# Kernel tuning notes

Measured on AMD Instinct MI355X. Metric: run time of the kernel, lower is better.

The kernel has to match this reference:

```python
import jax, jax.numpy as jnp
import numpy as np

B, T, F_, H1, H2, HEADS = 64, 128, 64, 32, 64, 4
E = H2 * F_  # embed_dim = hidden_dims[-1] * feats = 4096


def conv2d(x, w, b):
    # x: [b,c,H,W], w: [o,c,kh,kw], SAME padding (kernel 3 -> pad 1)
    y = jax.lax.conv_general_dilated(x, w, (1, 1), 'SAME',
                                     dimension_numbers=('NCHW', 'OIHW', 'NCHW'))
    return y + b[None, :, None, None]


def gru_layer(xs, h0, wg, bg, wc, bc):
    # xs: [b,t,c,H,W]; h0: [b,h,H,W]. Standard ConvGRU cell:
    #   r,u = sigmoid(conv([x,h])); cand = tanh(conv([x, r*h]))
    #   h' = (1-u)*h + u*cand
    def step(h, x):
        g = conv2d(jnp.concatenate([x, h], axis=1), wg, bg)
        r, u = jnp.split(jax.nn.sigmoid(g), 2, axis=1)
        cand = jnp.tanh(conv2d(jnp.concatenate([x, r * h], axis=1), wc, bc))
        h_next = (1.0 - u) * h + u * cand
        return h_next, h_next
    hT, ys = jax.lax.scan(step, h0, jnp.swapaxes(xs, 0, 1))
    return jnp.swapaxes(ys, 0, 1), hT  # [b,t,h,H,W], [b,h,H,W]


def mha(q, k, v, w_qkv, b_qkv, w_out, b_out):
    # q: [b,1,E], k/v: [b,t,E]; torch nn.MultiheadAttention (eval, no dropout)
    wq, wk, wv = jnp.split(w_qkv, 3, axis=0)
    bq, bk, bv = jnp.split(b_qkv, 3, axis=0)
    dh = E // HEADS
    def heads(x, w, bb):
        y = x @ w.T + bb
        b_, l_, _ = y.shape
        return y.reshape(b_, l_, HEADS, dh).transpose(0, 2, 1, 3)  # [b,h,l,dh]
    qh, kh, vh = heads(q, wq, bq), heads(k, wk, bk), heads(v, wv, bv)
    scores = jnp.einsum('bhqd,bhkd->bhqk', qh, kh) / jnp.sqrt(jnp.float32(dh))
    attn = jax.nn.softmax(scores, axis=-1)
    ctx = jnp.einsum('bhqk,bhkd->bhqd', attn, vh)
    ctx = ctx.transpose(0, 2, 1, 3).reshape(q.shape[0], q.shape[1], E)
    return ctx @ w_out.T + b_out


def setup_inputs() -> dict:
    key = jax.random.key(0)
    ks = jax.random.split(key, 24)
    s = 0.05
    d = {'x': jax.random.normal(ks[0], (B, T, F_), dtype=jnp.float32)}
    # encoder layer 0: in=1, h=H1; layer 1: in=H1, h=H2
    d['wg_e0'] = jax.random.normal(ks[1], (2 * H1, 1 + H1, 3, 3)) * s
    d['bg_e0'] = jnp.zeros((2 * H1,))
    d['wc_e0'] = jax.random.normal(ks[2], (H1, 1 + H1, 3, 3)) * s
    d['bc_e0'] = jnp.zeros((H1,))
    d['wg_e1'] = jax.random.normal(ks[3], (2 * H2, H1 + H2, 3, 3)) * s
    d['bg_e1'] = jnp.zeros((2 * H2,))
    d['wc_e1'] = jax.random.normal(ks[4], (H2, H1 + H2, 3, 3)) * s
    d['bc_e1'] = jnp.zeros((H2,))
    # decoder: input dim = 2*H2; hidden dims reversed [H2, H1]
    d['wg_d0'] = jax.random.normal(ks[5], (2 * H2, 2 * H2 + H2, 3, 3)) * s
    d['bg_d0'] = jnp.zeros((2 * H2,))
    d['wc_d0'] = jax.random.normal(ks[6], (H2, 2 * H2 + H2, 3, 3)) * s
    d['bc_d0'] = jnp.zeros((H2,))
    d['wg_d1'] = jax.random.normal(ks[7], (2 * H1, H2 + H1, 3, 3)) * s
    d['bg_d1'] = jnp.zeros((2 * H1,))
    d['wc_d1'] = jax.random.normal(ks[8], (H1, H2 + H1, 3, 3)) * s
    d['bc_d1'] = jnp.zeros((H1,))
    d['w_qkv'] = jax.random.normal(ks[9], (3 * E, E)) * (1.0 / np.sqrt(E))
    d['b_qkv'] = jnp.zeros((3 * E,))
    d['w_out'] = jax.random.normal(ks[10], (E, E)) * (1.0 / np.sqrt(E))
    d['b_out'] = jnp.zeros((E,))
    d['w_fin'] = jax.random.normal(ks[11], (1, H1, 1, 1)) * s
    d['b_fin'] = jnp.zeros((1,))
    return d


def reference(x, wg_e0, bg_e0, wc_e0, bc_e0, wg_e1, bg_e1, wc_e1, bc_e1,
              wg_d0, bg_d0, wc_d0, bc_d0, wg_d1, bg_d1, wc_d1, bc_d1,
              w_qkv, b_qkv, w_out, b_out, w_fin, b_fin):
    b, t, f = x.shape
    xr = x.reshape(b, t, 1, f, 1)
    # encoder (2 ConvGRU layers, zero init states)
    y0, h0 = gru_layer(xr, jnp.zeros((b, H1, f, 1), x.dtype), wg_e0, bg_e0, wc_e0, bc_e0)
    y1, h1 = gru_layer(y0, jnp.zeros((b, H2, f, 1), x.dtype), wg_e1, bg_e1, wc_e1, bc_e1)
    # attention bottleneck: query = last hidden, memory = encoder outputs
    query = h1.reshape(b, 1, E)
    memory = y1.reshape(b, t, E)
    context = mha(query, memory, memory, w_qkv, b_qkv, w_out, b_out)  # [b,1,E]
    ctx = context.reshape(b, 1, H2, f, 1)
    dec_in = jnp.concatenate([y1, jnp.broadcast_to(ctx, (b, t, H2, f, 1))], axis=2)
    # decoder init states: encoder last states reversed -> [h1 (H2), h0 (H1)]
    z0, _ = gru_layer(dec_in, h1, wg_d0, bg_d0, wc_d0, bc_d0)
    z1, _ = gru_layer(z0, h0, wg_d1, bg_d1, wc_d1, bc_d1)  # [b,t,H1,f,1]
    # final 1x1 conv applied per timestep == channel contraction
    rec = jnp.einsum('btcfw,oc->btofw', z1, w_fin[:, :, 0, 0]) + b_fin[None, None, :, None, None]
    return rec.reshape(b, t, f)
```

## Files before the change

kernel.cpp:

```cpp
#include <hip/hip_runtime.h>
#include <cstdint>


#define B_  64
#define T_  128
#define TC  32
#define NCH 4

__device__ __forceinline__ float wsum(float v) {
#pragma unroll
  for (int m = 32; m > 0; m >>= 1) v += __shfl_xor(v, m, 64);
  return v;
}
__device__ __forceinline__ float wmaxr(float v) {
#pragma unroll
  for (int m = 32; m > 0; m >>= 1) v = fmaxf(v, __shfl_xor(v, m, 64));
  return v;
}
__device__ __forceinline__ float sigmoidf_(float x) {
  return 1.f / (1.f + __expf(-x));
}
__device__ __forceinline__ float tanhf_(float x) {
  x = fminf(fmaxf(x, -15.f), 15.f);
  float e2 = __expf(2.f * x);
  return (e2 - 1.f) / (e2 + 1.f);
}

struct PackArgs {
  const float* src[16];
  float* dst[16];
  int intot[16];
  int ic0[16];
  int icn[16];
  int oc[16];
};

__global__ __launch_bounds__(256) void pack_all_kernel(PackArgs pa) {
  const int j = blockIdx.y;
  const int icN = pa.icn[j];
  const int total = pa.oc[j] * icN * 3;
  const int i = blockIdx.x * 256 + threadIdx.x;
  if (i >= total) return;
  const int per_oc = icN * 3;
  const int oc = i / per_oc;
  const int rem = i - oc * per_oc;
  const int ic = rem / 3, dk = rem - ic * 3;
  pa.dst[j][i] =
      pa.src[j][((size_t)(oc * pa.intot[j] + pa.ic0[j] + ic) * 3 + dk) * 3 + 1];
}

template <int INC, int OG, int OCC>
__device__ __forceinline__ void conv_x_body(
    float (*sin_)[72], int tid, int btl,
    const float* __restrict__ seq, int seqC, size_t sB,
    const float* __restrict__ ctx,
    const float* __restrict__ Wgx, const float* __restrict__ Wcx,
    const float* __restrict__ bg, const float* __restrict__ bc,
    float* __restrict__ out) {
  constexpr int OCT = OG + OCC;
  constexpr int NJ = OG / 32;
  constexpr int NJC = OCC / 32;
  const int b = btl >> 5;
  const int tl = btl & 31;
  const int ocg = tid >> 3;
  const int f0 = (tid & 7) << 3;

  for (int idx = tid; idx < INC * 72; idx += 256) {
    int ic = idx / 72, ff = idx - ic * 72;
    float v = 0.f;
    if (ff >= 1 && ff <= 64) {
      int fs = ff - 1;
      v = (ic < seqC)
              ? seq[(size_t)b * sB + (size_t)tl * seqC * 64 + ic * 64 + fs]
              : ctx[((size_t)b * (INC - seqC) + (ic - seqC)) * 64 + fs];
    }
    sin_[ic][ff] = v;
  }
  __syncthreads();

  if constexpr (INC >= 4) {
    {
      float acc[NJ][8];
#pragma unroll
      for (int j = 0; j < NJ; ++j) {
        float bb = bg[ocg + 32 * j];
#pragma unroll
        for (int ff = 0; ff < 8; ++ff) acc[j][ff] = bb;
      }
      for (int ic0 = 0; ic0 < INC; ic0 += 4) {
        float hv[4][10];
#pragma unroll
        for (int q = 0; q < 4; ++q) {
          float4 a4 = *(const float4*)&sin_[ic0 + q][f0];
          float4 b4 = *(const float4*)&sin_[ic0 + q][f0 + 4];
          float2 c2 = *(const float2*)&sin_[ic0 + q][f0 + 8];
          hv[q][0] = a4.x; hv[q][1] = a4.y; hv[q][2] = a4.z; hv[q][3] = a4.w;
          hv[q][4] = b4.x; hv[q][5] = b4.y; hv[q][6] = b4.z; hv[q][7] = b4.w;
          hv[q][8] = c2.x; hv[q][9] = c2.y;
        }
#pragma unroll
        for (int j = 0; j < NJ; ++j) {
          const int oc = ocg + 32 * j;
          const float4* w4 = (const float4*)(Wgx + ((size_t)oc * INC + ic0) * 3);
          float4 wa = w4[0], wb = w4[1], wc4 = w4[2];
          const float wt[12] = {wa.x, wa.y, wa.z, wa.w, wb.x, wb.y, wb.z, wb.w,
                                wc4.x, wc4.y, wc4.z, wc4.w};
#pragma unroll
          for (int q = 0; q < 4; ++q) {
            const float w0 = wt[3 * q], w1 = wt[3 * q + 1], w2 = wt[3 * q + 2];
#pragma unroll
            for (int ff = 0; ff < 8; ++ff)
              acc[j][ff] = fmaf(w0, hv[q][ff], fmaf(w1, hv[q][ff + 1], fmaf(w2, hv[q][ff + 2], acc[j][ff])));
          }
        }
      }
#pragma unroll
      for (int j = 0; j < NJ; ++j) {
        float* dst = out + ((size_t)btl * OCT + ocg + 32 * j) * 64 + f0;
        *(float4*)dst = make_float4(acc[j][0], acc[j][1], acc[j][2], acc[j][3]);
        *(float4*)(dst + 4) = make_float4(acc[j][4], acc[j][5], acc[j][6], acc[j][7]);
      }
    }
    {
      float acc[NJC][8];
#pragma unroll
      for (int j = 0; j < NJC; ++j) {
        float bb = bc[ocg + 32 * j];
#pragma unroll
        for (int ff = 0; ff < 8; ++ff) acc[j][ff] = bb;
      }
      for (int ic0 = 0; ic0 < INC; ic0 += 4) {
        float hv[4][10];
#pragma unroll
        for (int q = 0; q < 4; ++q) {
          float4 a4 = *(const float4*)&sin_[ic0 + q][f0];
          float4 b4 = *(const float4*)&sin_[ic0 + q][f0 + 4];
          float2 c2 = *(const float2*)&sin_[ic0 + q][f0 + 8];
          hv[q][0] = a4.x; hv[q][1] = a4.y; hv[q][2] = a4.z; hv[q][3] = a4.w;
          hv[q][4] = b4.x; hv[q][5] = b4.y; hv[q][6] = b4.z; hv[q][7] = b4.w;
          hv[q][8] = c2.x; hv[q][9] = c2.y;
        }
#pragma unroll
        for (int j = 0; j < NJC; ++j) {
          const int oc = ocg + 32 * j;
          const float4* w4 = (const float4*)(Wcx + ((size_t)oc * INC + ic0) * 3);
          float4 wa = w4[0], wb = w4[1], wc4 = w4[2];
          const float wt[12] = {wa.x, wa.y, wa.z, wa.w, wb.x, wb.y, wb.z, wb.w,
                                wc4.x, wc4.y, wc4.z, wc4.w};
#pragma unroll
          for (int q = 0; q < 4; ++q) {
            const float w0 = wt[3 * q], w1 = wt[3 * q + 1], w2 = wt[3 * q + 2];
#pragma unroll
            for (int ff = 0; ff < 8; ++ff)
              acc[j][ff] = fmaf(w0, hv[q][ff], fmaf(w1, hv[q][ff + 1], fmaf(w2, hv[q][ff + 2], acc[j][ff])));
          }
        }
      }
#pragma unroll
      for (int j = 0; j < NJC; ++j) {
        float* dst = out + ((size_t)btl * OCT + OG + ocg + 32 * j) * 64 + f0;
        *(float4*)dst = make_float4(acc[j][0], acc[j][1], acc[j][2], acc[j][3]);
        *(float4*)(dst + 4) = make_float4(acc[j][4], acc[j][5], acc[j][6], acc[j][7]);
      }
    }
  } else {
    float hv[10];
    {
      float4 a4 = *(const float4*)&sin_[0][f0];
      float4 b4 = *(const float4*)&sin_[0][f0 + 4];
      float2 c2 = *(const float2*)&sin_[0][f0 + 8];
      hv[0] = a4.x; hv[1] = a4.y; hv[2] = a4.z; hv[3] = a4.w;
      hv[4] = b4.x; hv[5] = b4.y; hv[6] = b4.z; hv[7] = b4.w;
      hv[8] = c2.x; hv[9] = c2.y;
    }
#pragma unroll
    for (int j = 0; j < NJ; ++j) {
      const int oc = ocg + 32 * j;
      const float w0 = Wgx[oc * 3], w1 = Wgx[oc * 3 + 1], w2 = Wgx[oc * 3 + 2];
      float acc[8];
#pragma unroll
      for (int ff = 0; ff < 8; ++ff)
        acc[ff] = fmaf(w0, hv[ff], fmaf(w1, hv[ff + 1], fmaf(w2, hv[ff + 2], bg[oc])));
      float* dst = out + ((size_t)btl * OCT + oc) * 64 + f0;
      *(float4*)dst = make_float4(acc[0], acc[1], acc[2], acc[3]);
      *(float4*)(dst + 4) = make_float4(acc[4], acc[5], acc[6], acc[7]);
    }
#pragma unroll
    for (int j = 0; j < NJC; ++j) {
      const int oc = ocg + 32 * j;
      const float w0 = Wcx[oc * 3], w1 = Wcx[oc * 3 + 1], w2 = Wcx[oc * 3 + 2];
      float acc[8];
#pragma unroll
      for (int ff = 0; ff < 8; ++ff)
        acc[ff] = fmaf(w0, hv[ff], fmaf(w1, hv[ff + 1], fmaf(w2, hv[ff + 2], bc[oc])));
      float* dst = out + ((size_t)btl * OCT + OG + oc) * 64 + f0;
      *(float4*)dst = make_float4(acc[0], acc[1], acc[2], acc[3]);
      *(float4*)(dst + 4) = make_float4(acc[4], acc[5], acc[6], acc[7]);
    }
  }
}

template <int INC, int OG, int OCC>
__global__ __launch_bounds__(256) void conv_x_kernel(
    const float* __restrict__ seq, int seqC, size_t sB,
    const float* __restrict__ ctx,
    const float* __restrict__ Wgx, const float* __restrict__ Wcx,
    const float* __restrict__ bg, const float* __restrict__ bc,
    float* __restrict__ out) {
  __shared__ float sin_[INC][72];
  conv_x_body<INC, OG, OCC>(sin_, threadIdx.x, blockIdx.x, seq, seqC, sB, ctx,
                            Wgx, Wcx, bg, bc, out);
}

__device__ __forceinline__ void final_body(
    int tid, int tile, const float* __restrict__ z1c,
    const float* __restrict__ wfin, const float* __restrict__ bfin,
    float* __restrict__ out, int tOff) {
  const int idx = tile * 256 + tid;
  const int f = idx & 63;
  const int tl = (idx >> 6) & 31;
  const int b = idx >> 11;
  const float* zp = z1c + ((size_t)b * TC + tl) * 2048 + f;
  float a = bfin[0];
#pragma unroll
  for (int c = 0; c < 32; ++c) a = fmaf(wfin[c], zp[c * 64], a);
  out[(size_t)b * 8192 + (size_t)(tOff + tl) * 64 + f] = a;
}

__global__ __launch_bounds__(256) void final_kernel(
    const float* __restrict__ z1c,
    const float* __restrict__ wfin, const float* __restrict__ bfin,
    float* __restrict__ out, int tOff) {
  final_body(threadIdx.x, blockIdx.x, z1c, wfin, bfin, out, tOff);
}

template <int HC>
__device__ __forceinline__ void gru_body(
    float* smem,
    const float* __restrict__ A, const float* __restrict__ Wgh,
    const float* __restrict__ Wch, const float* hinit,
    float* __restrict__ Y, size_t yB, float* hfinal, int b) {
  constexpr int NR = HC / 32;
  constexpr int OG = 2 * HC;
  constexpr int OCT = 3 * HC;
  float(*Hs)[68] = (float(*)[68])smem;
  float(*Rs)[68] = (float(*)[68])(smem + HC * 68);
  const int tid = threadIdx.x;
  const int ocg = tid >> 4;
  const int f0 = (tid & 15) << 2;
  const int im = (f0 == 0) ? 0 : f0 - 1;
  const bool lo = (f0 == 0), hi = (f0 == 60);

  float hreg[NR][4];
#pragma unroll
  for (int r = 0; r < NR; ++r) {
    const int oc = ocg + 32 * r;
    const float4 v = *(const float4*)(hinit + ((size_t)b * HC + oc) * 64 + f0);
    hreg[r][0] = v.x; hreg[r][1] = v.y; hreg[r][2] = v.z; hreg[r][3] = v.w;
    *(float4*)&Hs[oc][f0] = v;
  }
  __syncthreads();
  __builtin_amdgcn_s_setprio(1);

  for (int tl = 0; tl < TC; ++tl) {
    const float* Abt = A + ((size_t)b * TC + tl) * (OCT * 64);
    float accr[NR][4], accu[NR][4], accc[NR][4];
#pragma unroll
    for (int r = 0; r < NR; ++r) {
      const int oc = ocg + 32 * r;
      const float4 vr = *(const float4*)(Abt + (size_t)oc * 64 + f0);
      const float4 vu = *(const float4*)(Abt + (size_t)(HC + oc) * 64 + f0);
      const float4 vc = *(const float4*)(Abt + (size_t)(OG + oc) * 64 + f0);
      accr[r][0] = vr.x; accr[r][1] = vr.y; accr[r][2] = vr.z; accr[r][3] = vr.w;
      accu[r][0] = vu.x; accu[r][1] = vu.y; accu[r][2] = vu.z; accu[r][3] = vu.w;
      accc[r][0] = vc.x; accc[r][1] = vc.y; accc[r][2] = vc.z; accc[r][3] = vc.w;
    }
#pragma unroll 2
    for (int hc0 = 0; hc0 < HC; hc0 += 4) {
      float hv[4][6];
#pragma unroll
      for (int q = 0; q < 4; ++q) {
        const float4 h4 = *(const float4*)&Hs[hc0 + q][f0];
        const float lf = Hs[hc0 + q][im];
        const float rt = Hs[hc0 + q][f0 + 4];
        hv[q][0] = lo ? 0.f : lf;
        hv[q][1] = h4.x; hv[q][2] = h4.y; hv[q][3] = h4.z; hv[q][4] = h4.w;
        hv[q][5] = hi ? 0.f : rt;
      }
#pragma unroll
      for (int r = 0; r < NR; ++r) {
        {
          const float4* w4 = (const float4*)(Wgh + ((size_t)(ocg + 32 * r) * HC + hc0) * 3);
          const float4 wa = w4[0], wb = w4[1], wc4 = w4[2];
          const float wt[12] = {wa.x, wa.y, wa.z, wa.w, wb.x, wb.y, wb.z, wb.w,
                                wc4.x, wc4.y, wc4.z, wc4.w};
#pragma unroll
          for (int q = 0; q < 4; ++q) {
            const float w0 = wt[3 * q], w1 = wt[3 * q + 1], w2 = wt[3 * q + 2];
#pragma unroll
            for (int ff = 0; ff < 4; ++ff)
              accr[r][ff] = fmaf(w0, hv[q][ff], fmaf(w1, hv[q][ff + 1], fmaf(w2, hv[q][ff + 2], accr[r][ff])));
          }
        }
        {
          const float4* w4 = (const float4*)(Wgh + ((size_t)(HC + ocg + 32 * r) * HC + hc0) * 3);
          const float4 wa = w4[0], wb = w4[1], wc4 = w4[2];
          const float wt[12] = {wa.x, wa.y, wa.z, wa.w, wb.x, wb.y, wb.z, wb.w,
                                wc4.x, wc4.y, wc4.z, wc4.w};
#pragma unroll
          for (int q = 0; q < 4; ++q) {
            const float w0 = wt[3 * q], w1 = wt[3 * q + 1], w2 = wt[3 * q + 2];
#pragma unroll
            for (int ff = 0; ff < 4; ++ff)
              accu[r][ff] = fmaf(w0, hv[q][ff], fmaf(w1, hv[q][ff + 1], fmaf(w2, hv[q][ff + 2], accu[r][ff])));
          }
        }
      }
    }
// ... 11 lines not shown
    __syncthreads();
#pragma unroll 2
    for (int hc0 = 0; hc0 < HC; hc0 += 4) {
      float hv[4][6];
#pragma unroll
      for (int q = 0; q < 4; ++q) {
        const float4 h4 = *(const float4*)&Rs[hc0 + q][f0];
        const float lf = Rs[hc0 + q][im];
        const float rt = Rs[hc0 + q][f0 + 4];
        hv[q][0] = lo ? 0.f : lf;
        hv[q][1] = h4.x; hv[q][2] = h4.y; hv[q][3] = h4.z; hv[q][4] = h4.w;
        hv[q][5] = hi ? 0.f : rt;
      }
#pragma unroll
      for (int r = 0; r < NR; ++r) {
        const float4* w4 = (const float4*)(Wch + ((size_t)(ocg + 32 * r) * HC + hc0) * 3);
        const float4 wa = w4[0], wb = w4[1], wc4 = w4[2];
        const float wt[12] = {wa.x, wa.y, wa.z, wa.w, wb.x, wb.y, wb.z, wb.w,
                              wc4.x, wc4.y, wc4.z, wc4.w};
#pragma unroll
        for (int q = 0; q < 4; ++q) {
          const float w0 = wt[3 * q], w1 = wt[3 * q + 1], w2 = wt[3 * q + 2];
#pragma unroll
          for (int ff = 0; ff < 4; ++ff)
            accc[r][ff] = fmaf(w0, hv[q][ff], fmaf(w1, hv[q][ff + 1], fmaf(w2, hv[q][ff + 2], accc[r][ff])));
        }
      }
    }
#pragma unroll
    for (int r = 0; r < NR; ++r) {
      const int oc = ocg + 32 * r;
      float4 yv;
#pragma unroll
      for (int ff = 0; ff < 4; ++ff) {
        const float cd = tanhf_(accc[r][ff]);
        const float hn = fmaf(uu[r][ff], cd - hreg[r][ff], hreg[r][ff]);
        hreg[r][ff] = hn;
        (&yv.x)[ff] = hn;
      }
      *(float4*)(Y + (size_t)b * yB + (size_t)tl * (HC * 64) + (size_t)oc * 64 + f0) = yv;
      *(float4*)&Hs[oc][f0] = yv;
    }
    __syncthreads();
  }
  __builtin_amdgcn_s_setprio(0);
#pragma unroll
  for (int r = 0; r < NR; ++r) {
    const int oc = ocg + 32 * r;
    *(float4*)(hfinal + ((size_t)b * HC + oc) * 64 + f0) =
        make_float4(hreg[r][0], hreg[r][1], hreg[r][2], hreg[r][3]);
  }
}

template <int HC>
__global__ __launch_bounds__(512) void gru_rec_kernel(
    const float* __restrict__ A, const float* __restrict__ Wgh,
    const float* __restrict__ Wch, const float* hinit,
    float* __restrict__ Y, size_t yB, float* hfinal) {
  __shared__ float smem[2 * HC * 68];
  gru_body<HC>(smem, A, Wgh, Wch, hinit, Y, yB, hfinal, blockIdx.x);
}

struct GruArgs {
  const float* A;
  const float* Wgh;
  const float* Wch;
  const float* hinit;
  float* Y;
  size_t yB;
  float* hfinal;
};

__global__ __launch_bounds__(512) void gru_fused_kernel(GruArgs g64, GruArgs g32) {
  __shared__ float smem[2 * 64 * 68];
  if (blockIdx.x < 64) {
    gru_body<64>(smem, g64.A, g64.Wgh, g64.Wch, g64.hinit, g64.Y, g64.yB,
                 g64.hfinal, blockIdx.x);
  } else {
    gru_body<32>(smem, g32.A, g32.Wgh, g32.Wch, g32.hinit, g32.Y, g32.yB,
                 g32.hfinal, blockIdx.x - 64);
  }
}

struct ConvJob {
  int kind;
  int nblk;
  const float* seq;
  int seqC;
  size_t sB;
  const float* ctx;
  const float* w0;
  const float* w1;
  const float* b0;
  const float* b1;
  float* out;
  int tOff;
};

struct MegaArgs {
  GruArgs g64;
  GruArgs g32;
  int ng64, ng32, njobs;
  ConvJob jobs[4];
};

__global__ __launch_bounds__(512) void mega_kernel(MegaArgs ma) {
  __shared__ float smem[18432];
  int bid = blockIdx.x;
  if (bid < ma.ng64) {
    gru_body<64>(smem, ma.g64.A, ma.g64.Wgh, ma.g64.Wch, ma.g64.hinit,
                 ma.g64.Y, ma.g64.yB, ma.g64.hfinal, bid);
    return;
  }
  bid -= ma.ng64;
  if (bid < ma.ng32) {
    gru_body<32>(smem, ma.g32.A, ma.g32.Wgh, ma.g32.Wch, ma.g32.hinit,
                 ma.g32.Y, ma.g32.yB, ma.g32.hfinal, bid);
    return;
  }
  bid -= ma.ng32;
  const int half = threadIdx.x >> 8;
  const int tid = threadIdx.x & 255;
#pragma unroll 1
  for (int j = 0; j < ma.njobs; ++j) {
    if (bid < ma.jobs[j].nblk) {
      const ConvJob cj = ma.jobs[j];
      const int tile = bid * 2 + half;
      if (cj.kind == 2) {
        conv_x_body<128, 128, 64>((float(*)[72])(smem + half * 128 * 72), tid,
                                  tile, cj.seq, cj.seqC, cj.sB, cj.ctx, cj.w0,
                                  cj.w1, cj.b0, cj.b1, cj.out);
      } else if (cj.kind == 3) {
        conv_x_body<64, 64, 32>((float(*)[72])(smem + half * 64 * 72), tid,
                                tile, cj.seq, cj.seqC, cj.sB, cj.ctx, cj.w0,
                                cj.w1, cj.b0, cj.b1, cj.out);
      } else {
        final_body(tid, tile, cj.seq, cj.w0, cj.b0, cj.out, cj.tOff);
      }
      return;
    }
    bid -= ma.jobs[j].nblk;
  }
}

template <bool WT>
__global__ __launch_bounds__(256) void gemm64_kernel(
    const float* __restrict__ W, int wrs,
    const float* __restrict__ X, int xrs,
    float* __restrict__ O, int ors,
    const float* __restrict__ bias, int K,
    int ebh, size_t hsW, size_t hsX, size_t hsO, size_t hsB) {
  int eb = blockIdx.x;
  if (ebh > 0) {
    int h = blockIdx.x / ebh;
    eb = blockIdx.x - h * ebh;
    W += h * hsW; X += h * hsX; O += h * hsO;
    if (bias) bias += h * hsB;
  }
  const int e0 = eb * 64;
  __shared__ float Xs[64][68];
  __shared__ float Ws[64][68];
  const int tb4 = (threadIdx.x & 15) << 2;
  const int te4 = (threadIdx.x >> 4) << 2;
  float acc[4][4] = {};
  for (int k0 = 0; k0 < K; k0 += 64) {
    {
      const int row = threadIdx.x >> 2;
      const int kq = (threadIdx.x & 3) << 4;
      const float* src = X + (size_t)row * xrs + k0 + kq;
#pragma unroll
      for (int q = 0; q < 4; ++q) {
        float4 v = *(const float4*)(src + (q << 2));
        Xs[kq + (q << 2) + 0][row] = v.x;
        Xs[kq + (q << 2) + 1][row] = v.y;
        Xs[kq + (q << 2) + 2][row] = v.z;
        Xs[kq + (q << 2) + 3][row] = v.w;
      }
    }
    if (!WT) {
      const int row = threadIdx.x >> 2;
      const int kq = (threadIdx.x & 3) << 4;
      const float* src = W + (size_t)(e0 + row) * wrs + k0 + kq;
#pragma unroll
      for (int q = 0; q < 4; ++q) {
        float4 v = *(const float4*)(src + (q << 2));
        Ws[kq + (q << 2) + 0][row] = v.x;
        Ws[kq + (q << 2) + 1][row] = v.y;
        Ws[kq + (q << 2) + 2][row] = v.z;
// ... 86 lines not shown
  const int e = eb * 256 + threadIdx.x;
  __shared__ float ap[4][128];
  for (int i = threadIdx.x; i < 512; i += 256)
    ap[i >> 7][i & 127] = attnp[(size_t)b * 512 + i];
  __syncthreads();
  float a0 = 0, a1 = 0, a2 = 0, a3 = 0;
  const float* mb = mem + (size_t)b * 128 * 4096 + e;
#pragma unroll 4
  for (int t = 0; t < 128; ++t) {
    float m = mb[(size_t)t * 4096];
    a0 = fmaf(ap[0][t], m, a0);
    a1 = fmaf(ap[1][t], m, a1);
    a2 = fmaf(ap[2][t], m, a2);
    a3 = fmaf(ap[3][t], m, a3);
  }
  wmem[((size_t)b * 4 + 0) * 4096 + e] = a0;
  wmem[((size_t)b * 4 + 1) * 4096 + e] = a1;
  wmem[((size_t)b * 4 + 2) * 4096 + e] = a2;
  wmem[((size_t)b * 4 + 3) * 4096 + e] = a3;
}

extern "C" void kernel_launch(void* const* d_in, const int* in_sizes, int n_in,
                              void* d_out, int out_size, void* d_ws, size_t ws_size,
                              hipStream_t stream) {
  (void)in_sizes; (void)n_in; (void)out_size;
  const float* x     = (const float*)d_in[0];
  const float* wg_e0 = (const float*)d_in[1];
  const float* bg_e0 = (const float*)d_in[2];
  const float* wc_e0 = (const float*)d_in[3];
  const float* bc_e0 = (const float*)d_in[4];
  const float* wg_e1 = (const float*)d_in[5];
  const float* bg_e1 = (const float*)d_in[6];
  const float* wc_e1 = (const float*)d_in[7];
  const float* bc_e1 = (const float*)d_in[8];
  const float* wg_d0 = (const float*)d_in[9];
  const float* bg_d0 = (const float*)d_in[10];
  const float* wc_d0 = (const float*)d_in[11];
  const float* bc_d0 = (const float*)d_in[12];
  const float* wg_d1 = (const float*)d_in[13];
  const float* bg_d1 = (const float*)d_in[14];
  const float* wc_d1 = (const float*)d_in[15];
  const float* bc_d1 = (const float*)d_in[16];
  const float* w_qkv = (const float*)d_in[17];
  const float* b_qkv = (const float*)d_in[18];
  const float* w_out = (const float*)d_in[19];
  const float* b_out = (const float*)d_in[20];
  const float* w_fin = (const float*)d_in[21];
  const float* b_fin = (const float*)d_in[22];
  float* out = (float*)d_out;

  float* WS = (float*)d_ws;
  size_t off = 0;
  auto alloc = [&](size_t n) { float* p = WS + off; off += (n + 63) & ~(size_t)63; return p; };
  float* Amp0 = alloc((size_t)B_ * TC * 192 * 64);
  float* A960 = alloc((size_t)B_ * TC * 96 * 64);
  float* Y0c  = alloc((size_t)B_ * TC * 32 * 64);
  float* Y1   = alloc((size_t)B_ * T_ * 64 * 64);
  float* Z0p[2] = {alloc((size_t)B_ * TC * 64 * 64), alloc((size_t)B_ * TC * 64 * 64)};
  float* Z1p0 = alloc((size_t)B_ * TC * 32 * 64);
  float* He0p[2] = {alloc((size_t)B_ * 32 * 64), alloc((size_t)B_ * 32 * 64)};
  float* He1p[2] = {alloc((size_t)B_ * 64 * 64), alloc((size_t)B_ * 64 * 64)};
  float* Hd0p[2] = {alloc((size_t)B_ * 64 * 64), alloc((size_t)B_ * 64 * 64)};
  float* Hd1p[2] = {alloc((size_t)B_ * 32 * 64), alloc((size_t)B_ * 32 * 64)};
  float* QBUF = alloc((size_t)B_ * 4096);
  float* QKH  = alloc((size_t)B_ * 4 * 4096);
  float* WMEM = alloc((size_t)B_ * 4 * 4096);
  float* CTXB = alloc((size_t)B_ * 4096);
  float* CTXO = alloc((size_t)B_ * 4096);
  float* SCR  = alloc((size_t)B_ * 4 * 128);
  float* ATTN = alloc((size_t)B_ * 4 * 128);
  float* wgx_e0 = alloc(64 * 1 * 3);    float* wgh_e0 = alloc(64 * 32 * 3);
  float* wcx_e0 = alloc(32 * 1 * 3);    float* wch_e0 = alloc(32 * 32 * 3);
  float* wgx_e1 = alloc(128 * 32 * 3);  float* wgh_e1 = alloc(128 * 64 * 3);
  float* wcx_e1 = alloc(64 * 32 * 3);   float* wch_e1 = alloc(64 * 64 * 3);
  float* wgx_d0 = alloc(128 * 128 * 3); float* wgh_d0 = alloc(128 * 64 * 3);
  float* wcx_d0 = alloc(64 * 128 * 3);  float* wch_d0 = alloc(64 * 64 * 3);
  float* wgx_d1 = alloc(64 * 64 * 3);   float* wgh_d1 = alloc(64 * 32 * 3);
  float* wcx_d1 = alloc(32 * 64 * 3);   float* wch_d1 = alloc(32 * 32 * 3);
  const size_t off_r9 = off;
  float* Amp1 = alloc((size_t)B_ * TC * 192 * 64);
  float* A961 = alloc((size_t)B_ * TC * 96 * 64);
  float* Z1p1 = alloc((size_t)B_ * TC * 32 * 64);
  const size_t off_full = off;
  if (ws_size < off_r9 * sizeof(float)) return;
  const bool mega_ok = (ws_size >= off_full * sizeof(float));

  float* Amp[2] = {Amp0, Amp1};
  float* A96p[2] = {A960, A961};
  float* Z1p[2] = {Z1p0, Z1p1};

  {
    PackArgs pa;
    const float* srcs[16] = {wg_e0, wg_e0, wc_e0, wc_e0, wg_e1, wg_e1, wc_e1, wc_e1,
                             wg_d0, wg_d0, wc_d0, wc_d0, wg_d1, wg_d1, wc_d1, wc_d1};
    float* dsts[16] = {wgx_e0, wgh_e0, wcx_e0, wch_e0, wgx_e1, wgh_e1, wcx_e1, wch_e1,
                       wgx_d0, wgh_d0, wcx_d0, wch_d0, wgx_d1, wgh_d1, wcx_d1, wch_d1};
    int intot[16] = {33, 33, 33, 33, 96, 96, 96, 96, 192, 192, 192, 192, 96, 96, 96, 96};
    int ic0[16]   = {0, 1, 0, 1, 0, 32, 0, 32, 0, 128, 0, 128, 0, 64, 0, 64};
    int icn[16]   = {1, 32, 1, 32, 32, 64, 32, 64, 128, 64, 128, 64, 64, 32, 64, 32};
    int occ[16]   = {64, 64, 32, 32, 128, 128, 64, 64, 128, 128, 64, 64, 64, 64, 32, 32};
    for (int j = 0; j < 16; ++j) {
      pa.src[j] = srcs[j]; pa.dst[j] = dsts[j];
      pa.intot[j] = intot[j]; pa.ic0[j] = ic0[j]; pa.icn[j] = icn[j]; pa.oc[j] = occ[j];
    }
    pack_all_kernel<<<dim3(192, 16), 256, 0, stream>>>(pa);
  }

  hipMemsetAsync(He0p[0], 0, (size_t)B_ * 32 * 64 * 4, stream);
  hipMemsetAsync(He1p[0], 0, (size_t)B_ * 64 * 64 * 4, stream);

  auto conv_e0 = [&](int c) {
    conv_x_kernel<1, 64, 32><<<2048, 256, 0, stream>>>(
        x + (size_t)c * TC * 64, 1, (size_t)T_ * 64, nullptr,
        wgx_e0, wcx_e0, bg_e0, bc_e0, A96p[0]);
  };
  auto conv_e1 = [&]() {
    conv_x_kernel<32, 128, 64><<<2048, 256, 0, stream>>>(
        Y0c, 32, (size_t)TC * 32 * 64, nullptr,
        wgx_e1, wcx_e1, bg_e1, bc_e1, Amp[0]);
  };

  conv_e0(0);
  gru_rec_kernel<32><<<64, 512, 0, stream>>>(
      A96p[0], wgh_e0, wch_e0, He0p[0], Y0c, (size_t)TC * 2048, He0p[1]);
  conv_e1();
  for (int c = 0; c < NCH; ++c) {
    GruArgs g64 = {Amp[0], wgh_e1, wch_e1, He1p[c & 1],
                   Y1 + (size_t)c * TC * 4096, (size_t)T_ * 4096, He1p[(c + 1) & 1]};
    if (c < NCH - 1) {
      conv_e0(c + 1);
      GruArgs g32 = {A96p[0], wgh_e0, wch_e0, He0p[(c + 1) & 1],
                     Y0c, (size_t)TC * 2048, He0p[c & 1]};
      gru_fused_kernel<<<128, 512, 0, stream>>>(g64, g32);
      conv_e1();
    } else {
      gru_rec_kernel<64><<<64, 512, 0, stream>>>(
          g64.A, g64.Wgh, g64.Wch, g64.hinit, g64.Y, g64.yB, g64.hfinal);
    }
  }
  float* He0f = He0p[0];
  float* He1f = He1p[0];

  const float* wq = w_qkv;
  const float* wk = w_qkv + (size_t)4096 * 4096;
  const float* wv = w_qkv + (size_t)8192 * 4096;
  gemm64_kernel<false><<<64, 256, 0, stream>>>(wq, 4096, He1f, 4096, QBUF, 4096,
                                               b_qkv, 4096, 0, 0, 0, 0, 0);
  gemm64_kernel<true><<<256, 256, 0, stream>>>(wk, 4096, QBUF, 4096, QKH, 16384,
                                               nullptr, 1024, 64,
                                               (size_t)1024 * 4096, 1024, 4096, 0);
  attn_scores_kernel<<<B_ * 16, 256, 0, stream>>>(QKH, Y1, SCR);
  attn_softmax_kernel<<<B_, 256, 0, stream>>>(SCR, QBUF, b_qkv, ATTN);
  attn_wsum_kernel<<<B_ * 16, 256, 0, stream>>>(ATTN, Y1, WMEM);
  gemm64_kernel<false><<<64, 256, 0, stream>>>(wv, 4096, WMEM, 16384, CTXB, 4096,
                                               b_qkv + 8192, 4096, 16,
                                               (size_t)1024 * 4096, 4096, 1024, 1024);
  gemm64_kernel<false><<<64, 256, 0, stream>>>(w_out, 4096, CTXB, 4096, CTXO, 4096,
                                               b_out, 4096, 0, 0, 0, 0, 0);

  if (mega_ok) {
    auto JD0 = [&](int c, float* dst) {
      ConvJob j{}; j.kind = 2; j.nblk = 1024;
      j.seq = Y1 + (size_t)c * TC * 4096; j.seqC = 64; j.sB = (size_t)T_ * 4096;
      j.ctx = CTXO; j.w0 = wgx_d0; j.w1 = wcx_d0; j.b0 = bg_d0; j.b1 = bc_d0;
      j.out = dst; return j;
    };
    auto JD1 = [&](float* z0src, float* dst) {
      ConvJob j{}; j.kind = 3; j.nblk = 1024;
      j.seq = z0src; j.seqC = 64; j.sB = (size_t)TC * 4096;
      j.ctx = nullptr; j.w0 = wgx_d1; j.w1 = wcx_d1; j.b0 = bg_d1; j.b1 = bc_d1;
      j.out = dst; return j;
    };
    auto JFIN = [&](float* z1src, int tOff) {
      ConvJob j{}; j.kind = 4; j.nblk = 256;
      j.seq = z1src; j.w0 = w_fin; j.b0 = b_fin; j.out = out; j.tOff = tOff;
      return j;
    };
    auto mega = [&](const GruArgs* a64, const GruArgs* a32, int nj,
                    const ConvJob* js) {
      MegaArgs ma{};
      ma.ng64 = a64 ? 64 : 0; if (a64) ma.g64 = *a64;
      ma.ng32 = a32 ? 64 : 0; if (a32) ma.g32 = *a32;
      ma.njobs = nj;
      int grid = ma.ng64 + ma.ng32;
      for (int i = 0; i < nj; ++i) { ma.jobs[i] = js[i]; grid += js[i].nblk; }
      mega_kernel<<<grid, 512, 0, stream>>>(ma);
    };

    GruArgs gd0[4], gd1[4];
    for (int c = 0; c < 4; ++c) {
      gd0[c] = {Amp[c & 1], wgh_d0, wch_d0,
                (c == 0 ? He1f : Hd0p[c & 1]),
                Z0p[c & 1], (size_t)TC * 4096, Hd0p[(c + 1) & 1]};
      gd1[c] = {A96p[c & 1], wgh_d1, wch_d1,
                (c == 0 ? He0f : Hd1p[c & 1]),
                Z1p[c & 1], (size_t)TC * 2048, Hd1p[(c + 1) & 1]};
    }

    conv_x_kernel<128, 128, 64><<<2048, 256, 0, stream>>>(
        Y1, 64, (size_t)T_ * 4096, CTXO, wgx_d0, wcx_d0, bg_d0, bc_d0, Amp[0]);
    { ConvJob js[1] = {JD0(1, Amp[1])};
      mega(&gd0[0], nullptr, 1, js); }
    { ConvJob js[2] = {JD1(Z0p[0], A96p[0]), JD0(2, Amp[0])};
      mega(&gd0[1], nullptr, 2, js); }
    { ConvJob js[2] = {JD1(Z0p[1], A96p[1]), JD0(3, Amp[1])};
      mega(&gd0[2], &gd1[0], 2, js); }
    { ConvJob js[2] = {JD1(Z0p[0], A96p[0]), JFIN(Z1p[0], 0)};
      mega(&gd0[3], &gd1[1], 2, js); }
    { ConvJob js[2] = {JD1(Z0p[1], A96p[1]), JFIN(Z1p[1], TC)};
      mega(nullptr, &gd1[2], 2, js); }
    { ConvJob js[1] = {JFIN(Z1p[0], 2 * TC)};
      mega(nullptr, &gd1[3], 1, js); }
    final_kernel<<<512, 256, 0, stream>>>(Z1p[1], w_fin, b_fin, out, 3 * TC);
  } else {
    auto conv_d0 = [&](int c) {
      conv_x_kernel<128, 128, 64><<<2048, 256, 0, stream>>>(
          Y1 + (size_t)c * TC * 4096, 64, (size_t)T_ * 4096, CTXO,
          wgx_d0, wcx_d0, bg_d0, bc_d0, Amp[0]);
    };
    auto conv_d1 = [&](int c) {
      conv_x_kernel<64, 64, 32><<<2048, 256, 0, stream>>>(
          Z0p[c & 1], 64, (size_t)TC * 4096, nullptr,
          wgx_d1, wcx_d1, bg_d1, bc_d1, A96p[0]);
    };
    conv_d0(0);
    gru_rec_kernel<64><<<64, 512, 0, stream>>>(
        Amp[0], wgh_d0, wch_d0, He1f, Z0p[0], (size_t)TC * 4096, Hd0p[1]);
    conv_d1(0);
    for (int c = 1; c < NCH; ++c) {
      conv_d0(c);
      GruArgs g64 = {Amp[0], wgh_d0, wch_d0, Hd0p[c & 1],
                     Z0p[c & 1], (size_t)TC * 4096, Hd0p[(c + 1) & 1]};
      GruArgs g32 = {A96p[0], wgh_d1, wch_d1,
                     (c - 1 == 0 ? He0f : Hd1p[(c - 1) & 1]),
                     Z1p[0], (size_t)TC * 2048, Hd1p[c & 1]};
      gru_fused_kernel<<<128, 512, 0, stream>>>(g64, g32);
      final_kernel<<<512, 256, 0, stream>>>(Z1p[0], w_fin, b_fin, out, (c - 1) * TC);
      conv_d1(c);
    }
    gru_rec_kernel<32><<<64, 512, 0, stream>>>(
        A96p[0], wgh_d1, wch_d1, Hd1p[1], Z1p[0], (size_t)TC * 2048, Hd1p[0]);
    final_kernel<<<512, 256, 0, stream>>>(Z1p[0], w_fin, b_fin, out, 3 * TC);
  }
}
```

Measured before the change: 7.725 ms.

## Halve time-chunk size and generalize mega-kernel pipeline over more chunks

Reduces the time chunk from 32 to 16 steps (8 chunks) and turns the hand-written decoder mega-kernel schedule into a generic software pipeline. GRU recurrence, input convolutions and the final projection of adjacent chunks now overlap in each launch. The encoder layer-0 input convolution is hoisted into one full-sequence launch, and buffers are double-buffered unconditionally. The aim is a shorter pipeline fill/drain so the serial GRU chain is less exposed, at the cost of more launches and a larger workspace requirement.

New measurement: 7.282 ms, median of 2. 1.06x faster.

```diff
diff --git a/kernel.cpp b/kernel.cpp
--- a/kernel.cpp
+++ b/kernel.cpp
@@ -4,8 +4,8 @@
 
 #define B_  64
 #define T_  128
-#define TC  32
-#define NCH 4
+#define TC  16
+#define NCH 8
 
 __device__ __forceinline__ float wsum(float v) {
 #pragma unroll
@@ -51,7 +51,7 @@
 
 template <int INC, int OG, int OCC>
 __device__ __forceinline__ void conv_x_body(
-    float (*sin_)[72], int tid, int btl,
+    float (*sin_)[72], int tid, int b, int tl, int oidx,
     const float* __restrict__ seq, int seqC, size_t sB,
     const float* __restrict__ ctx,
     const float* __restrict__ Wgx, const float* __restrict__ Wcx,
@@ -60,8 +60,6 @@
   constexpr int OCT = OG + OCC;
   constexpr int NJ = OG / 32;
   constexpr int NJC = OCC / 32;
-  const int b = btl >> 5;
-  const int tl = btl & 31;
   const int ocg = tid >> 3;
   const int f0 = (tid & 7) << 3;
 
@@ -116,7 +114,7 @@
       }
 #pragma unroll
       for (int j = 0; j < NJ; ++j) {
-        float* dst = out + ((size_t)btl * OCT + ocg + 32 * j) * 64 + f0;
+        float* dst = out + ((size_t)oidx * OCT + ocg + 32 * j) * 64 + f0;
         *(float4*)dst = make_float4(acc[j][0], acc[j][1], acc[j][2], acc[j][3]);
         *(float4*)(dst + 4) = make_float4(acc[j][4], acc[j][5], acc[j][6], acc[j][7]);
       }
@@ -158,7 +156,7 @@
       }
 #pragma unroll
       for (int j = 0; j < NJC; ++j) {
-        float* dst = out + ((size_t)btl * OCT + OG + ocg + 32 * j) * 64 + f0;
+        float* dst = out + ((size_t)oidx * OCT + OG + ocg + 32 * j) * 64 + f0;
         *(float4*)dst = make_float4(acc[j][0], acc[j][1], acc[j][2], acc[j][3]);
         *(float4*)(dst + 4) = make_float4(acc[j][4], acc[j][5], acc[j][6], acc[j][7]);
       }
@@ -181,7 +179,7 @@
 #pragma unroll
       for (int ff = 0; ff < 8; ++ff)
         acc[ff] = fmaf(w0, hv[ff], fmaf(w1, hv[ff + 1], fmaf(w2, hv[ff + 2], bg[oc])));
-      float* dst = out + ((size_t)btl * OCT + oc) * 64 + f0;
+      float* dst = out + ((size_t)oidx * OCT + oc) * 64 + f0;
       *(float4*)dst = make_float4(acc[0], acc[1], acc[2], acc[3]);
       *(float4*)(dst + 4) = make_float4(acc[4], acc[5], acc[6], acc[7]);
     }
@@ -193,7 +191,7 @@
 #pragma unroll
       for (int ff = 0; ff < 8; ++ff)
         acc[ff] = fmaf(w0, hv[ff], fmaf(w1, hv[ff + 1], fmaf(w2, hv[ff + 2], bc[oc])));
-      float* dst = out + ((size_t)btl * OCT + OG + oc) * 64 + f0;
+      float* dst = out + ((size_t)oidx * OCT + OG + oc) * 64 + f0;
       *(float4*)dst = make_float4(acc[0], acc[1], acc[2], acc[3]);
       *(float4*)(dst + 4) = make_float4(acc[4], acc[5], acc[6], acc[7]);
     }
@@ -206,10 +204,12 @@
     const float* __restrict__ ctx,
     const float* __restrict__ Wgx, const float* __restrict__ Wcx,
     const float* __restrict__ bg, const float* __restrict__ bc,
-    float* __restrict__ out) {
+    float* __restrict__ out, int tdiv) {
   __shared__ float sin_[INC][72];
-  conv_x_body<INC, OG, OCC>(sin_, threadIdx.x, blockIdx.x, seq, seqC, sB, ctx,
-                            Wgx, Wcx, bg, bc, out);
+  const int b = blockIdx.x / tdiv;
+  const int tl = blockIdx.x - b * tdiv;
+  conv_x_body<INC, OG, OCC>(sin_, threadIdx.x, b, tl, blockIdx.x, seq, seqC,
+                            sB, ctx, Wgx, Wcx, bg, bc, out);
 }
 
 __device__ __forceinline__ void final_body(
@@ -218,8 +218,8 @@
     float* __restrict__ out, int tOff) {
   const int idx = tile * 256 + tid;
   const int f = idx & 63;
-  const int tl = (idx >> 6) & 31;
-  const int b = idx >> 11;
+  const int tl = (idx >> 6) & (TC - 1);
+  const int b = idx >> 10;
   const float* zp = z1c + ((size_t)b * TC + tl) * 2048 + f;
   float a = bfin[0];
 #pragma unroll
@@ -237,8 +237,9 @@
 template <int HC>
 __device__ __forceinline__ void gru_body(
     float* smem,
-    const float* __restrict__ A, const float* __restrict__ Wgh,
-    const float* __restrict__ Wch, const float* hinit,
+    const float* __restrict__ A, size_t aB,
+    const float* __restrict__ Wgh, const float* __restrict__ Wch,
+    const float* hinit,
     float* __restrict__ Y, size_t yB, float* hfinal, int b) {
   constexpr int NR = HC / 32;
   constexpr int OG = 2 * HC;
@@ -263,7 +264,7 @@
   __builtin_amdgcn_s_setprio(1);
 
   for (int tl = 0; tl < TC; ++tl) {
-    const float* Abt = A + ((size_t)b * TC + tl) * (OCT * 64);
+    const float* Abt = A + (size_t)b * aB + (size_t)tl * (OCT * 64);
     float accr[NR][4], accu[NR][4], accc[NR][4];
 #pragma unroll
     for (int r = 0; r < NR; ++r) {
@@ -381,17 +382,9 @@
   }
 }
 
-template <int HC>
-__global__ __launch_bounds__(512) void gru_rec_kernel(
-    const float* __restrict__ A, const float* __restrict__ Wgh,
-    const float* __restrict__ Wch, const float* hinit,
-    float* __restrict__ Y, size_t yB, float* hfinal) {
-  __shared__ float smem[2 * HC * 68];
-  gru_body<HC>(smem, A, Wgh, Wch, hinit, Y, yB, hfinal, blockIdx.x);
-}
-
 struct GruArgs {
   const float* A;
+  size_t aB;
   const float* Wgh;
   const float* Wch;
   const float* hinit;
@@ -400,14 +393,21 @@
   float* hfinal;
 };
 
+template <int HC>
+__global__ __launch_bounds__(512) void gru_rec_kernel(GruArgs g) {
+  __shared__ float smem[2 * HC * 68];
+  gru_body<HC>(smem, g.A, g.aB, g.Wgh, g.Wch, g.hinit, g.Y, g.yB, g.hfinal,
+               blockIdx.x);
+}
+
 __global__ __launch_bounds__(512) void gru_fused_kernel(GruArgs g64, GruArgs g32) {
   __shared__ float smem[2 * 64 * 68];
   if (blockIdx.x < 64) {
-    gru_body<64>(smem, g64.A, g64.Wgh, g64.Wch, g64.hinit, g64.Y, g64.yB,
-                 g64.hfinal, blockIdx.x);
+    gru_body<64>(smem, g64.A, g64.aB, g64.Wgh, g64.Wch, g64.hinit, g64.Y,
+                 g64.yB, g64.hfinal, blockIdx.x);
   } else {
-    gru_body<32>(smem, g32.A, g32.Wgh, g32.Wch, g32.hinit, g32.Y, g32.yB,
-                 g32.hfinal, blockIdx.x - 64);
+    gru_body<32>(smem, g32.A, g32.aB, g32.Wgh, g32.Wch, g32.hinit, g32.Y,
+                 g32.yB, g32.hfinal, blockIdx.x - 64);
   }
 }
 
@@ -437,14 +437,14 @@
   __shared__ float smem[18432];
   int bid = blockIdx.x;
   if (bid < ma.ng64) {
-    gru_body<64>(smem, ma.g64.A, ma.g64.Wgh, ma.g64.Wch, ma.g64.hinit,
-                 ma.g64.Y, ma.g64.yB, ma.g64.hfinal, bid);
+    gru_body<64>(smem, ma.g64.A, ma.g64.aB, ma.g64.Wgh, ma.g64.Wch,
+                 ma.g64.hinit, ma.g64.Y, ma.g64.yB, ma.g64.hfinal, bid);
     return;
   }
   bid -= ma.ng64;
   if (bid < ma.ng32) {
-    gru_body<32>(smem, ma.g32.A, ma.g32.Wgh, ma.g32.Wch, ma.g32.hinit,
-                 ma.g32.Y, ma.g32.yB, ma.g32.hfinal, bid);
+    gru_body<32>(smem, ma.g32.A, ma.g32.aB, ma.g32.Wgh, ma.g32.Wch,
+                 ma.g32.hinit, ma.g32.Y, ma.g32.yB, ma.g32.hfinal, bid);
     return;
   }
   bid -= ma.ng32;
@@ -455,14 +455,16 @@
     if (bid < ma.jobs[j].nblk) {
       const ConvJob cj = ma.jobs[j];
       const int tile = bid * 2 + half;
+      const int b = tile >> 4;
+      const int tl = tile & (TC - 1);
       if (cj.kind == 2) {
         conv_x_body<128, 128, 64>((float(*)[72])(smem + half * 128 * 72), tid,
-                                  tile, cj.seq, cj.seqC, cj.sB, cj.ctx, cj.w0,
-                                  cj.w1, cj.b0, cj.b1, cj.out);
+                                  b, tl, tile, cj.seq, cj.seqC, cj.sB, cj.ctx,
+                                  cj.w0, cj.w1, cj.b0, cj.b1, cj.out);
       } else if (cj.kind == 3) {
         conv_x_body<64, 64, 32>((float(*)[72])(smem + half * 64 * 72), tid,
-                                tile, cj.seq, cj.seqC, cj.sB, cj.ctx, cj.w0,
-                                cj.w1, cj.b0, cj.b1, cj.out);
+                                b, tl, tile, cj.seq, cj.seqC, cj.sB, cj.ctx,
+                                cj.w0, cj.w1, cj.b0, cj.b1, cj.out);
       } else {
         final_body(tid, tile, cj.seq, cj.w0, cj.b0, cj.out, cj.tOff);
       }
@@ -655,12 +657,13 @@
   float* WS = (float*)d_ws;
   size_t off = 0;
   auto alloc = [&](size_t n) { float* p = WS + off; off += (n + 63) & ~(size_t)63; return p; };
-  float* Amp0 = alloc((size_t)B_ * TC * 192 * 64);
-  float* A960 = alloc((size_t)B_ * TC * 96 * 64);
-  float* Y0c  = alloc((size_t)B_ * TC * 32 * 64);
+  float* Amp[2] = {alloc((size_t)B_ * TC * 192 * 64), alloc((size_t)B_ * TC * 192 * 64)};
+  float* A96full = alloc((size_t)B_ * T_ * 96 * 64);
+  float* A96d[2] = {alloc((size_t)B_ * TC * 96 * 64), alloc((size_t)B_ * TC * 96 * 64)};
+  float* Y0p[2] = {alloc((size_t)B_ * TC * 32 * 64), alloc((size_t)B_ * TC * 32 * 64)};
   float* Y1   = alloc((size_t)B_ * T_ * 64 * 64);
   float* Z0p[2] = {alloc((size_t)B_ * TC * 64 * 64), alloc((size_t)B_ * TC * 64 * 64)};
-  float* Z1p0 = alloc((size_t)B_ * TC * 32 * 64);
+  float* Z1p[2] = {alloc((size_t)B_ * TC * 32 * 64), alloc((size_t)B_ * TC * 32 * 64)};
   float* He0p[2] = {alloc((size_t)B_ * 32 * 64), alloc((size_t)B_ * 32 * 64)};
   float* He1p[2] = {alloc((size_t)B_ * 64 * 64), alloc((size_t)B_ * 64 * 64)};
   float* Hd0p[2] = {alloc((size_t)B_ * 64 * 64), alloc((size_t)B_ * 64 * 64)};
@@ -680,17 +683,7 @@
   float* wcx_d0 = alloc(64 * 128 * 3);  float* wch_d0 = alloc(64 * 64 * 3);
   float* wgx_d1 = alloc(64 * 64 * 3);   float* wgh_d1 = alloc(64 * 32 * 3);
   float* wcx_d1 = alloc(32 * 64 * 3);   float* wch_d1 = alloc(32 * 32 * 3);
-  const size_t off_r9 = off;
-  float* Amp1 = alloc((size_t)B_ * TC * 192 * 64);
-  float* A961 = alloc((size_t)B_ * TC * 96 * 64);
-  float* Z1p1 = alloc((size_t)B_ * TC * 32 * 64);
-  const size_t off_full = off;
-  if (ws_size < off_r9 * sizeof(float)) return;
-  const bool mega_ok = (ws_size >= off_full * sizeof(float));
-
-  float* Amp[2] = {Amp0, Amp1};
-  float* A96p[2] = {A960, A961};
-  float* Z1p[2] = {Z1p0, Z1p1};
+  if (ws_size < off * sizeof(float)) return;
 
   {
     PackArgs pa;
@@ -712,33 +705,34 @@
   hipMemsetAsync(He0p[0], 0, (size_t)B_ * 32 * 64 * 4, stream);
   hipMemsetAsync(He1p[0], 0, (size_t)B_ * 64 * 64 * 4, stream);
 
-  auto conv_e0 = [&](int c) {
-    conv_x_kernel<1, 64, 32><<<2048, 256, 0, stream>>>(
-        x + (size_t)c * TC * 64, 1, (size_t)T_ * 64, nullptr,
-        wgx_e0, wcx_e0, bg_e0, bc_e0, A96p[0]);
+  conv_x_kernel<1, 64, 32><<<B_ * T_, 256, 0, stream>>>(
+      x, 1, (size_t)T_ * 64, nullptr, wgx_e0, wcx_e0, bg_e0, bc_e0,
+      A96full, T_);
+
+  auto g32e = [&](int c) {
+    GruArgs g{A96full + (size_t)c * TC * 96 * 64, (size_t)T_ * 96 * 64,
+              wgh_e0, wch_e0, He0p[c & 1], Y0p[c & 1], (size_t)TC * 2048,
+              He0p[(c + 1) & 1]};
+    return g;
   };
-  auto conv_e1 = [&]() {
-    conv_x_kernel<32, 128, 64><<<2048, 256, 0, stream>>>(
-        Y0c, 32, (size_t)TC * 32 * 64, nullptr,
-        wgx_e1, wcx_e1, bg_e1, bc_e1, Amp[0]);
+  auto conv_e1 = [&](int c) {
+    conv_x_kernel<32, 128, 64><<<B_ * TC, 256, 0, stream>>>(
+        Y0p[c & 1], 32, (size_t)TC * 2048, nullptr,
+        wgx_e1, wcx_e1, bg_e1, bc_e1, Amp[c & 1], TC);
   };
 
-  conv_e0(0);
-  gru_rec_kernel<32><<<64, 512, 0, stream>>>(
-      A96p[0], wgh_e0, wch_e0, He0p[0], Y0c, (size_t)TC * 2048, He0p[1]);
-  conv_e1();
+  { GruArgs g = g32e(0); gru_rec_kernel<32><<<64, 512, 0, stream>>>(g); }
+  conv_e1(0);
   for (int c = 0; c < NCH; ++c) {
-    GruArgs g64 = {Amp[0], wgh_e1, wch_e1, He1p[c & 1],
-                   Y1 + (size_t)c * TC * 4096, (size_t)T_ * 4096, He1p[(c + 1) & 1]};
+    GruArgs g64 = {Amp[c & 1], (size_t)TC * 192 * 64, wgh_e1, wch_e1,
+                   He1p[c & 1], Y1 + (size_t)c * TC * 4096, (size_t)T_ * 4096,
+                   He1p[(c + 1) & 1]};
     if (c < NCH - 1) {
-      conv_e0(c + 1);
-      GruArgs g32 = {A96p[0], wgh_e0, wch_e0, He0p[(c + 1) & 1],
-                     Y0c, (size_t)TC * 2048, He0p[c & 1]};
+      GruArgs g32 = g32e(c + 1);
       gru_fused_kernel<<<128, 512, 0, stream>>>(g64, g32);
-      conv_e1();
+      conv_e1(c + 1);
     } else {
-      gru_rec_kernel<64><<<64, 512, 0, stream>>>(
-          g64.A, g64.Wgh, g64.Wch, g64.hinit, g64.Y, g64.yB, g64.hfinal);
+      gru_rec_kernel<64><<<64, 512, 0, stream>>>(g64);
     }
   }
   float* He0f = He0p[0];
@@ -761,88 +755,59 @@
   gemm64_kernel<false><<<64, 256, 0, stream>>>(w_out, 4096, CTXB, 4096, CTXO, 4096,
                                                b_out, 4096, 0, 0, 0, 0, 0);
 
-  if (mega_ok) {
-    auto JD0 = [&](int c, float* dst) {
-      ConvJob j{}; j.kind = 2; j.nblk = 1024;
-      j.seq = Y1 + (size_t)c * TC * 4096; j.seqC = 64; j.sB = (size_t)T_ * 4096;
-      j.ctx = CTXO; j.w0 = wgx_d0; j.w1 = wcx_d0; j.b0 = bg_d0; j.b1 = bc_d0;
-      j.out = dst; return j;
-    };
-    auto JD1 = [&](float* z0src, float* dst) {
-      ConvJob j{}; j.kind = 3; j.nblk = 1024;
-      j.seq = z0src; j.seqC = 64; j.sB = (size_t)TC * 4096;
-      j.ctx = nullptr; j.w0 = wgx_d1; j.w1 = wcx_d1; j.b0 = bg_d1; j.b1 = bc_d1;
-      j.out = dst; return j;
-    };
-    auto JFIN = [&](float* z1src, int tOff) {
-      ConvJob j{}; j.kind = 4; j.nblk = 256;
-      j.seq = z1src; j.w0 = w_fin; j.b0 = b_fin; j.out = out; j.tOff = tOff;
-      return j;
-    };
-    auto mega = [&](const GruArgs* a64, const GruArgs* a32, int nj,
-                    const ConvJob* js) {
-      MegaArgs ma{};
-      ma.ng64 = a64 ? 64 : 0; if (a64) ma.g64 = *a64;
-      ma.ng32 = a32 ? 64 : 0; if (a32) ma.g32 = *a32;
-      ma.njobs = nj;
-      int grid = ma.ng64 + ma.ng32;
-      for (int i = 0; i < nj; ++i) { ma.jobs[i] = js[i]; grid += js[i].nblk; }
-      mega_kernel<<<grid, 512, 0, stream>>>(ma);
-    };
-
-    GruArgs gd0[4], gd1[4];
-    for (int c = 0; c < 4; ++c) {
-      gd0[c] = {Amp[c & 1], wgh_d0, wch_d0,
-                (c == 0 ? He1f : Hd0p[c & 1]),
-                Z0p[c & 1], (size_t)TC * 4096, Hd0p[(c + 1) & 1]};
-      gd1[c] = {A96p[c & 1], wgh_d1, wch_d1,
-                (c == 0 ? He0f : Hd1p[c & 1]),
-                Z1p[c & 1], (size_t)TC * 2048, Hd1p[(c + 1) & 1]};
-    }
-
-    conv_x_kernel<128, 128, 64><<<2048, 256, 0, stream>>>(
-        Y1, 64, (size_t)T_ * 4096, CTXO, wgx_d0, wcx_d0, bg_d0, bc_d0, Amp[0]);
-    { ConvJob js[1] = {JD0(1, Amp[1])};
-      mega(&gd0[0], nullptr, 1, js); }
-    { ConvJob js[2] = {JD1(Z0p[0], A96p[0]), JD0(2, Amp[0])};
-      mega(&gd0[1], nullptr, 2, js); }
-    { ConvJob js[2] = {JD1(Z0p[1], A96p[1]), JD0(3, Amp[1])};
-      mega(&gd0[2], &gd1[0], 2, js); }
-    { ConvJob js[2] = {JD1(Z0p[0], A96p[0]), JFIN(Z1p[0], 0)};
-      mega(&gd0[3], &gd1[1], 2, js); }
-    { ConvJob js[2] = {JD1(Z0p[1], A96p[1]), JFIN(Z1p[1], TC)};
-      mega(nullptr, &gd1[2], 2, js); }
-    { ConvJob js[1] = {JFIN(Z1p[0], 2 * TC)};
-      mega(nullptr, &gd1[3], 1, js); }
-    final_kernel<<<512, 256, 0, stream>>>(Z1p[1], w_fin, b_fin, out, 3 * TC);
-  } else {
-    auto conv_d0 = [&](int c) {
-      conv_x_kernel<128, 128, 64><<<2048, 256, 0, stream>>>(
-          Y1 + (size_t)c * TC * 4096, 64, (size_t)T_ * 4096, CTXO,
-          wgx_d0, wcx_d0, bg_d0, bc_d0, Amp[0]);
-    };
-    auto conv_d1 = [&](int c) {
-      conv_x_kernel<64, 64, 32><<<2048, 256, 0, stream>>>(
-          Z0p[c & 1], 64, (size_t)TC * 4096, nullptr,
-          wgx_d1, wcx_d1, bg_d1, bc_d1, A96p[0]);
-    };
-    conv_d0(0);
-    gru_rec_kernel<64><<<64, 512, 0, stream>>>(
-        Amp[0], wgh_d0, wch_d0, He1f, Z0p[0], (size_t)TC * 4096, Hd0p[1]);
-    conv_d1(0);
-    for (int c = 1; c < NCH; ++c) {
-      conv_d0(c);
-      GruArgs g64 = {Amp[0], wgh_d0, wch_d0, Hd0p[c & 1],
-                     Z0p[c & 1], (size_t)TC * 4096, Hd0p[(c + 1) & 1]};
-      GruArgs g32 = {A96p[0], wgh_d1, wch_d1,
-                     (c - 1 == 0 ? He0f : Hd1p[(c - 1) & 1]),
-                     Z1p[0], (size_t)TC * 2048, Hd1p[c & 1]};
-      gru_fused_kernel<<<128, 512, 0, stream>>>(g64, g32);
-      final_kernel<<<512, 256, 0, stream>>>(Z1p[0], w_fin, b_fin, out, (c - 1) * TC);
-      conv_d1(c);
-    }
-    gru_rec_kernel<32><<<64, 512, 0, stream>>>(
-        A96p[0], wgh_d1, wch_d1, Hd1p[1], Z1p[0], (size_t)TC * 2048, Hd1p[0]);
-    final_kernel<<<512, 256, 0, stream>>>(Z1p[0], w_fin, b_fin, out, 3 * TC);
-  }
-}
+  auto JD0 = [&](int c, float* dst) {
+    ConvJob j{}; j.kind = 2; j.nblk = B_ * TC / 2;
+    j.seq = Y1 + (size_t)c * TC * 4096; j.seqC = 64; j.sB = (size_t)T_ * 4096;
+    j.ctx = CTXO; j.w0 = wgx_d0; j.w1 = wcx_d0; j.b0 = bg_d0; j.b1 = bc_d0;
+    j.out = dst; return j;
+  };
+  auto JD1 = [&](float* z0src, float* dst) {
+    ConvJob j{}; j.kind = 3; j.nblk = B_ * TC / 2;
+    j.seq = z0src; j.seqC = 64; j.sB = (size_t)TC * 4096;
+    j.ctx = nullptr; j.w0 = wgx_d1; j.w1 = wcx_d1; j.b0 = bg_d1; j.b1 = bc_d1;
+    j.out = dst; return j;
+  };
+  auto JFIN = [&](float* z1src, int tOff) {
+    ConvJob j{}; j.kind = 4; j.nblk = B_ * TC * 64 / 512;
+    j.seq = z1src; j.w0 = w_fin; j.b0 = b_fin; j.out = out; j.tOff = tOff;
+    return j;
+  };
+  auto mega = [&](const GruArgs* a64, const GruArgs* a32, int nj,
+                  const ConvJob* js) {
+    MegaArgs ma{};
+    ma.ng64 = a64 ? 64 : 0; if (a64) ma.g64 = *a64;
+    ma.ng32 = a32 ? 64 : 0; if (a32) ma.g32 = *a32;
+    ma.njobs = nj;
+    int grid = ma.ng64 + ma.ng32;
+    for (int i = 0; i < nj; ++i) { ma.jobs[i] = js[i]; grid += js[i].nblk; }
+    mega_kernel<<<grid, 512, 0, stream>>>(ma);
+  };
+
+  GruArgs gd0[NCH], gd1[NCH];
+  for (int c = 0; c < NCH; ++c) {
+    gd0[c] = {Amp[c & 1], (size_t)TC * 192 * 64, wgh_d0, wch_d0,
+              (c == 0 ? He1f : Hd0p[c & 1]),
+              Z0p[c & 1], (size_t)TC * 4096, Hd0p[(c + 1) & 1]};
+    gd1[c] = {A96d[c & 1], (size_t)TC * 96 * 64, wgh_d1, wch_d1,
+              (c == 0 ? He0f : Hd1p[c & 1]),
+              Z1p[c & 1], (size_t)TC * 2048, Hd1p[(c + 1) & 1]};
+  }
+
+  conv_x_kernel<128, 128, 64><<<B_ * TC, 256, 0, stream>>>(
+      Y1, 64, (size_t)T_ * 4096, CTXO, wgx_d0, wcx_d0, bg_d0, bc_d0,
+      Amp[0], TC);
+  for (int k = 0; k <= NCH + 1; ++k) {
+    const GruArgs* a64 = (k <= NCH - 1) ? &gd0[k] : nullptr;
+    const GruArgs* a32 = (k >= 2 && k - 2 <= NCH - 1) ? &gd1[k - 2] : nullptr;
+    ConvJob js[4];
+    int nj = 0;
+    if (k + 1 <= NCH - 1) js[nj++] = JD0(k + 1, Amp[(k + 1) & 1]);
+    if (k >= 1 && k - 1 <= NCH - 1)
+      js[nj++] = JD1(Z0p[(k - 1) & 1], A96d[(k - 1) & 1]);
+    if (k >= 3 && k - 3 <= NCH - 1)
+      js[nj++] = JFIN(Z1p[(k - 3) & 1], (k - 3) * TC);
+    mega(a64, a32, nj, js);
+  }
+  final_kernel<<<B_ * TC * 64 / 256, 256, 0, stream>>>(
+      Z1p[(NCH - 1) & 1], w_fin, b_fin, out, (NCH - 1) * TC);
+}
```
